# Kernel optimization log

Measured on AMD Instinct MI355X. Metric: run time of the kernel, lower is better.

The kernel has to match this reference:

```python
import jax, jax.numpy as jnp
import numpy as np
from jax import lax


def setup_inputs() -> dict:
    key = jax.random.key(0)
    k1, k2 = jax.random.split(key)
    B, C, H, W = 4, 64, 64, 64
    foreground = jax.random.normal(k1, (B, C, H, W), dtype=jnp.float32)
    masks = jax.random.uniform(k2, (B, 1, H, W), dtype=jnp.float32)
    return {"foreground": foreground, "masks": masks}


def reference(foreground, masks):
    # First-call path of KnowledgeConsistentAttention (att_scores_prev is None).
    # patch_size=3 -> padding=1 around 1x1 dynamic kernels; propagate_size=3 -> 3x3 sum pool.
    B, C, H, W = foreground.shape
    P = H * W
    # Dynamic 1x1 kernels: one per spatial location, L2-normalized over channels.
    K = foreground.reshape(B, C, P).transpose(0, 2, 1)            # [B, P, C]
    norm = jnp.sqrt(jnp.sum(K * K, axis=2, keepdims=True))        # flatten(1).norm per kernel
    K = K / (norm + 1e-8)
    # conv2d with 1x1 kernels and padding=1 == GEMM over zero-padded input.
    Xpad = jnp.pad(foreground, ((0, 0), (0, 0), (1, 1), (1, 1)))  # [B, C, H+2, W+2]
    scores = jnp.einsum('bpc,bchw->bphw', K, Xpad)                # [B, P, H+2, W+2]
    # avg_pool2d(k=3, stride=1, pad=1) * 9 == zero-padded 3x3 sum pool.
    scores = lax.reduce_window(scores, jnp.float32(0.0), lax.add,
                               (1, 1, 3, 3), (1, 1, 1, 1), 'SAME')
    attn = jax.nn.softmax(scores, axis=1)                          # softmax over P kernels
    # conv_transpose2d with 1x1 kernels, padding=1 crops the border back to HxW.
    out = jnp.einsum('bphw,bpc->bchw', attn[:, :, 1:-1, 1:-1], K)  # [B, C, H, W]
    return out
```

## Files before the change

kernel.cpp:

```cpp
#include <hip/hip_runtime.h>
#include <hip/hip_bf16.h>
#include <math.h>

#define Bn 4
#define Cn 64
#define Pn 4096
#define QT 32
#define PBK 128
#define NITER (Pn / PBK)
#define LOG2E 1.4426950408889634f

typedef __attribute__((ext_vector_type(8))) short short8;
typedef __attribute__((ext_vector_type(4))) float float4v;
typedef unsigned short bfu;

__device__ __forceinline__ bfu f2bf(float x) {
    unsigned u = __float_as_uint(x);
    u = (u + 0x7fffu + ((u >> 16) & 1u)) >> 16;
    return (bfu)u;
}

__device__ __forceinline__ void async_load16(const bfu* g, bfu* l) {
    __builtin_amdgcn_global_load_lds(
        (const __attribute__((address_space(1))) unsigned int*)(const void*)g,
        (__attribute__((address_space(3))) unsigned int*)(void*)l,
        16, 0, 0);
}

__global__ __launch_bounds__(256) void prep_kernel(const float* __restrict__ fg,
                                                   bfu* __restrict__ Kpc,
                                                   bfu* __restrict__ Kcp,
                                                   float* __restrict__ S) {
    __shared__ float shbuf[64 * 64];
    int t = threadIdx.x;
    if (blockIdx.x < 512) {
        float* tile  = shbuf;
        float* rnorm = shbuf + 64 * 33;
        int b  = blockIdx.x >> 7;
        int p0 = (blockIdx.x & 127) << 5;
        const float* src = fg + (size_t)b * Cn * Pn + p0;
        #pragma unroll
        for (int i = 0; i < 8; ++i) {
            int idx = i * 256 + t;
            int c = idx >> 5, p = idx & 31;
            tile[c * 33 + p] = src[(size_t)c * Pn + p];
        }
        __syncthreads();
        if (t < 32) {
            float ss = 0.f;
            #pragma unroll
            for (int c = 0; c < 64; ++c) { float v = tile[c * 33 + t]; ss += v * v; }
            rnorm[t] = 1.0f / (sqrtf(ss) + 1e-8f);
        }
        __syncthreads();
        bfu* dpc = Kpc + ((size_t)b * Pn + p0) * Cn;
        #pragma unroll
        for (int i = 0; i < 8; ++i) {
            int idx = i * 256 + t;
            int p = idx >> 6, c = idx & 63;
            dpc[(size_t)p * Cn + c] = f2bf(tile[c * 33 + p] * rnorm[p]);
        }
        bfu* dcp = Kcp + (size_t)b * Cn * Pn + p0;
        #pragma unroll
        for (int i = 0; i < 8; ++i) {
            int idx = i * 256 + t;
            int c = idx >> 5, p = idx & 31;
            dcp[(size_t)c * Pn + p] = f2bf(tile[c * 33 + p] * rnorm[p]);
        }
    } else {
        float (*pl)[64] = (float(*)[64])shbuf;
        int bc = blockIdx.x - 512;
        const float* src = fg + (size_t)bc * Pn;
        float*       dst = S  + (size_t)bc * Pn;
        #pragma unroll
        for (int i = 0; i < 16; ++i) {
            int idx = i * 256 + t;
            pl[idx >> 6][idx & 63] = src[idx];
        }
        __syncthreads();
        #pragma unroll
        for (int i = 0; i < 16; ++i) {
            int idx = i * 256 + t;
            int h = idx >> 6, w = idx & 63;
            float s = 0.f;
            #pragma unroll
            for (int dh = -1; dh <= 1; ++dh) {
                int hh = h + dh;
                if (hh < 0 || hh >= 64) continue;
                #pragma unroll
                for (int dw = -1; dw <= 1; ++dw) {
                    int ww = w + dw;
                    if (ww < 0 || ww >= 64) continue;
                    s += pl[hh][ww];
                }
            }
            dst[idx] = s * LOG2E;
        }
    }
}

__global__ __launch_bounds__(512, 4) void flash_kernel(const bfu* __restrict__ Kpc,
                                                       const bfu* __restrict__ Kcp,
                                                       const float* __restrict__ S,
                                                       float* __restrict__ out) {
    __shared__ __align__(16) bfu smem[26624];
    __shared__ float wredl[8][QT];
    bfu* Sl = smem + 16384;

    int b  = blockIdx.x >> 7;
    int q0 = (blockIdx.x & 127) * QT;
    int t  = threadIdx.x;
    int w = t >> 6, l = t & 63, lq = l & 15, quad = l >> 4;
    int cw = w & 1;
    int kq = w >> 1;

    const float* Sg  = S   + (size_t)b * Cn * Pn;
    const bfu*   gpc = Kpc + (size_t)b * Pn * Cn;
    const bfu*   gcp = Kcp + (size_t)b * Cn * Pn;

    {
        int c = t >> 3, qq = (t & 7) * 4;
        const float* sp = &Sg[(size_t)c * Pn + q0 + qq];
        float4 v0 = *(const float4*)sp;
        float vv[4] = {v0.x, v0.y, v0.z, v0.w};
        int ch = c >> 3, cl = c & 7;
        #pragma unroll
        for (int i = 0; i < 4; ++i) {
            int row = qq + i;
            Sl[row * 64 + ((ch ^ (row & 7)) << 3) + cl] = f2bf(vv[i]);
        }
    }

    #pragma unroll
    for (int pb0 = 0; pb0 < 2; ++pb0) {
        const bfu* gsrc = gpc + (size_t)pb0 * PBK * Cn;
        #pragma unroll
        for (int j = 0; j < 2; ++j) {
            int g = j * 8 + w;
            int ci = g * 64 + l;
            int row = ci >> 3, chp = ci & 7;
            async_load16(gsrc + (size_t)row * Cn + ((chp ^ (row & 7)) << 3),
                         smem + pb0 * 8192 + g * 512);
        }
    }
    __syncthreads();

    short8 bs[2][2];
    #pragma unroll
    for (int nt = 0; nt < 2; ++nt)
        #pragma unroll
        for (int ks = 0; ks < 2; ++ks) {
            int row = nt * 16 + lq;
            bs[nt][ks] = *(const short8*)&Sl[row * 64 + (((ks * 4 + quad) ^ (lq & 7)) << 3)];
        }

    float4v o[2][2];
    #pragma unroll
    for (int ct = 0; ct < 2; ++ct)
        #pragma unroll
        for (int nt = 0; nt < 2; ++nt) o[ct][nt] = (float4v){0.f, 0.f, 0.f, 0.f};
    float lacc[2] = {0.f, 0.f};

    for (int pb = 0; pb < NITER; ++pb) {
        bfu* KpcC = smem + (pb & 1) * 8192;
        bfu* ElC  = smem + 18432 + (pb & 1) * 4096;

        float4 akr[2];
        #pragma unroll
        for (int ct = 0; ct < 2; ++ct)
            akr[ct] = *(const float4*)&gcp[(size_t)(32 * cw + 16 * ct + lq) * Pn +
                                           pb * PBK + 32 * kq + quad * 8];

        short8 af[2];
        #pragma unroll
        for (int ks = 0; ks < 2; ++ks) {
            int row = w * 16 + lq;
            af[ks] = *(const short8*)&KpcC[row * 64 + (((ks * 4 + quad) ^ (lq & 7)) << 3)];
        }
        float4v sc[2];
        #pragma unroll
        for (int nt = 0; nt < 2; ++nt) {
            float4v acc = (float4v){0.f, 0.f, 0.f, 0.f};
            acc = __builtin_amdgcn_mfma_f32_16x16x32_bf16(af[0], bs[nt][0], acc, 0, 0, 0);
            acc = __builtin_amdgcn_mfma_f32_16x16x32_bf16(af[1], bs[nt][1], acc, 0, 0, 0);
            sc[nt] = acc;
        }

        #pragma unroll
        for (int nt = 0; nt < 2; ++nt) {
            int row = nt * 16 + lq;
            float e0 = __builtin_amdgcn_exp2f(sc[nt][0]);
            float e1 = __builtin_amdgcn_exp2f(sc[nt][1]);
            float e2 = __builtin_amdgcn_exp2f(sc[nt][2]);
            float e3 = __builtin_amdgcn_exp2f(sc[nt][3]);
            lacc[nt] += (e0 + e1) + (e2 + e3);
            __hip_bfloat162 h01 = __float22bfloat162_rn(make_float2(e0, e1));
            __hip_bfloat162 h23 = __float22bfloat162_rn(make_float2(e2, e3));
            uint2 pk = make_uint2(*(unsigned*)&h01, *(unsigned*)&h23);
            int col = w * 16 + quad * 4;
            int ch = (col >> 3) ^ (row & 15), cl = col & 7;
            *(uint2*)&ElC[row * PBK + ch * 8 + cl] = pk;
        }

        __syncthreads();

        if (pb + 2 < NITER) {
            const bfu* gsrc = gpc + (size_t)(pb + 2) * PBK * Cn;
            #pragma unroll
            for (int j = 0; j < 2; ++j) {
                int g = j * 8 + w;
                int ci = g * 64 + l;
                int row = ci >> 3, chp = ci & 7;
                async_load16(gsrc + (size_t)row * Cn + ((chp ^ (row & 7)) << 3),
                             KpcC + g * 512);
            }
        }

        #pragma unroll
        for (int ct = 0; ct < 2; ++ct) {
            short8 ak = *(short8*)&akr[ct];
            #pragma unroll
            for (int nt = 0; nt < 2; ++nt) {
                int rowB = nt * 16 + lq;
                short8 bk = *(const short8*)&ElC[rowB * PBK + (((4 * kq + quad) ^ (rowB & 15)) << 3)];
                o[ct][nt] = __builtin_amdgcn_mfma_f32_16x16x32_bf16(ak, bk, o[ct][nt], 0, 0, 0);
            }
        }
    }

    #pragma unroll
    for (int nt = 0; nt < 2; ++nt) {
        lacc[nt] += __shfl_xor(lacc[nt], 16);
        lacc[nt] += __shfl_xor(lacc[nt], 32);
    }
    if (quad == 0) { wredl[w][lq] = lacc[0]; wredl[w][16 + lq] = lacc[1]; }

    float* Ol = (float*)smem;
    __syncthreads();
    #pragma unroll
    for (int ct = 0; ct < 2; ++ct)
        #pragma unroll
        for (int nt = 0; nt < 2; ++nt)
            #pragma unroll
            for (int r = 0; r < 4; ++r)
                Ol[(kq * 64 + cw * 32 + ct * 16 + quad * 4 + r) * 33 + nt * 16 + lq] = o[ct][nt][r];
    __syncthreads();
    float* og = out + (size_t)b * Cn * Pn;
    #pragma unroll
    for (int i = 0; i < 4; ++i) {
        int idx = i * 512 + t;
        int c = idx >> 5, q = idx & 31;
        float lsum = ((wredl[0][q] + wredl[1][q]) + (wredl[2][q] + wredl[3][q])) +
                     ((wredl[4][q] + wredl[5][q]) + (wredl[6][q] + wredl[7][q]));
        float v = ((Ol[c * 33 + q] + Ol[(64 + c) * 33 + q]) +
                   (Ol[(128 + c) * 33 + q] + Ol[(192 + c) * 33 + q])) / lsum;
        og[(size_t)c * Pn + q0 + q] = v;
    }
}

extern "C" void kernel_launch(void* const* d_in, const int* in_sizes, int n_in,
                              void* d_out, int out_size, void* d_ws, size_t ws_size,
                              hipStream_t stream) {
    const float* fg = (const float*)d_in[0];
    float* out = (float*)d_out;
    bfu*   Kpc = (bfu*)d_ws;
    bfu*   Kcp = Kpc + (size_t)Bn * Pn * Cn;
    float* S   = (float*)(Kcp + (size_t)Bn * Pn * Cn);

    prep_kernel <<<768, 256, 0, stream>>>(fg, Kpc, Kcp, S);
    flash_kernel<<<Bn * 128, 512, 0, stream>>>(Kpc, Kcp, S, out);
}
```

Before: 107.1 us.

## Keep exp tile in registers and feed PV MFMA directly, dropping LDS round trip

The second GEMM is restructured so each wave uses its own exponentiated score fragment directly as the A operand of 16x16x16 MFMAs, removing the per-iteration LDS write of the probability tile and the block-wide barrier. K in [P,C] is now read straight from global into registers. A transposed, tiled copy of K (16-position blocks of 64x16) is streamed into per-wave LDS slots with async loads, waited on via s_waitcnt. Each wave now produces partial outputs over its own P slice, so the epilogue does a two-phase LDS reduction across waves. This trades barrier and LDS traffic for more accumulators and a heavier final reduction.

Measured after the change: 105.8 us. Within noise of the previous version (-1.2%).

```diff
diff --git a/kernel.cpp b/kernel.cpp
--- a/kernel.cpp
+++ b/kernel.cpp
@@ -11,6 +11,7 @@
 #define LOG2E 1.4426950408889634f
 
 typedef __attribute__((ext_vector_type(8))) short short8;
+typedef __attribute__((ext_vector_type(4))) short short4v;
 typedef __attribute__((ext_vector_type(4))) float float4v;
 typedef unsigned short bfu;
 
@@ -29,7 +30,7 @@
 
 __global__ __launch_bounds__(256) void prep_kernel(const float* __restrict__ fg,
                                                    bfu* __restrict__ Kpc,
-                                                   bfu* __restrict__ Kcp,
+                                                   bfu* __restrict__ Kcp2,
                                                    float* __restrict__ S) {
     __shared__ float shbuf[64 * 64];
     int t = threadIdx.x;
@@ -60,12 +61,13 @@
             int p = idx >> 6, c = idx & 63;
             dpc[(size_t)p * Cn + c] = f2bf(tile[c * 33 + p] * rnorm[p]);
         }
-        bfu* dcp = Kcp + (size_t)b * Cn * Pn + p0;
+        bfu* d2 = Kcp2 + ((size_t)b * 256 + (p0 >> 4)) * 1024;
         #pragma unroll
         for (int i = 0; i < 8; ++i) {
             int idx = i * 256 + t;
             int c = idx >> 5, p = idx & 31;
-            dcp[(size_t)c * Pn + p] = f2bf(tile[c * 33 + p] * rnorm[p]);
+            d2[(size_t)(p >> 4) * 1024 + c * 16 + (p & 15)] =
+                f2bf(tile[c * 33 + p] * rnorm[p]);
         }
     } else {
         float (*pl)[64] = (float(*)[64])shbuf;
@@ -100,10 +102,10 @@
 }
 
 __global__ __launch_bounds__(512, 4) void flash_kernel(const bfu* __restrict__ Kpc,
-                                                       const bfu* __restrict__ Kcp,
+                                                       const bfu* __restrict__ Kcp2,
                                                        const float* __restrict__ S,
                                                        float* __restrict__ out) {
-    __shared__ __align__(16) bfu smem[26624];
+    __shared__ __align__(16) bfu smem[18432];
     __shared__ float wredl[8][QT];
     bfu* Sl = smem + 16384;
 
@@ -111,12 +113,10 @@
     int q0 = (blockIdx.x & 127) * QT;
     int t  = threadIdx.x;
     int w = t >> 6, l = t & 63, lq = l & 15, quad = l >> 4;
-    int cw = w & 1;
-    int kq = w >> 1;
-
-    const float* Sg  = S   + (size_t)b * Cn * Pn;
-    const bfu*   gpc = Kpc + (size_t)b * Pn * Cn;
-    const bfu*   gcp = Kcp + (size_t)b * Cn * Pn;
+
+    const float* Sg  = S    + (size_t)b * Cn * Pn;
+    const bfu*   gpc = Kpc  + (size_t)b * Pn * Cn;
+    const bfu*   gt  = Kcp2 + (size_t)b * 256 * 1024;
 
     {
         int c = t >> 3, qq = (t & 7) * 4;
@@ -131,17 +131,11 @@
         }
     }
 
-    #pragma unroll
-    for (int pb0 = 0; pb0 < 2; ++pb0) {
-        const bfu* gsrc = gpc + (size_t)pb0 * PBK * Cn;
-        #pragma unroll
-        for (int j = 0; j < 2; ++j) {
-            int g = j * 8 + w;
-            int ci = g * 64 + l;
-            int row = ci >> 3, chp = ci & 7;
-            async_load16(gsrc + (size_t)row * Cn + ((chp ^ (row & 7)) << 3),
-                         smem + pb0 * 8192 + g * 512);
-        }
+    {
+        const bfu* src = gt + (size_t)w * 1024 + l * 8;
+        bfu* dst = smem + w * 1024;
+        async_load16(src, dst);
+        async_load16(src + 512, dst + 512);
     }
     __syncthreads();
 
@@ -154,77 +148,57 @@
             bs[nt][ks] = *(const short8*)&Sl[row * 64 + (((ks * 4 + quad) ^ (lq & 7)) << 3)];
         }
 
-    float4v o[2][2];
-    #pragma unroll
-    for (int ct = 0; ct < 2; ++ct)
-        #pragma unroll
-        for (int nt = 0; nt < 2; ++nt) o[ct][nt] = (float4v){0.f, 0.f, 0.f, 0.f};
+    float4v o[2][4];
+    #pragma unroll
+    for (int nt = 0; nt < 2; ++nt)
+        #pragma unroll
+        for (int cb = 0; cb < 4; ++cb) o[nt][cb] = (float4v){0.f, 0.f, 0.f, 0.f};
     float lacc[2] = {0.f, 0.f};
 
     for (int pb = 0; pb < NITER; ++pb) {
-        bfu* KpcC = smem + (pb & 1) * 8192;
-        bfu* ElC  = smem + 18432 + (pb & 1) * 4096;
-
-        float4 akr[2];
-        #pragma unroll
-        for (int ct = 0; ct < 2; ++ct)
-            akr[ct] = *(const float4*)&gcp[(size_t)(32 * cw + 16 * ct + lq) * Pn +
-                                           pb * PBK + 32 * kq + quad * 8];
-
-        short8 af[2];
-        #pragma unroll
-        for (int ks = 0; ks < 2; ++ks) {
-            int row = w * 16 + lq;
-            af[ks] = *(const short8*)&KpcC[row * 64 + (((ks * 4 + quad) ^ (lq & 7)) << 3)];
-        }
+        bfu* tile = smem + (pb & 1) * 8192 + w * 1024;
+
+        const bfu* ap = gpc + ((size_t)pb * PBK + 16 * w + lq) * Cn + quad * 8;
+        float4 a0 = *(const float4*)ap;
+        float4 a1 = *(const float4*)(ap + 32);
+
+        if (pb + 1 < NITER) {
+            const bfu* src = gt + ((size_t)(pb + 1) * 8 + w) * 1024 + l * 8;
+            bfu* dst = smem + ((pb + 1) & 1) * 8192 + w * 1024;
+            async_load16(src, dst);
+            async_load16(src + 512, dst + 512);
+        }
+
+        short8 af0 = *(short8*)&a0, af1 = *(short8*)&a1;
         float4v sc[2];
         #pragma unroll
         for (int nt = 0; nt < 2; ++nt) {
             float4v acc = (float4v){0.f, 0.f, 0.f, 0.f};
-            acc = __builtin_amdgcn_mfma_f32_16x16x32_bf16(af[0], bs[nt][0], acc, 0, 0, 0);
-            acc = __builtin_amdgcn_mfma_f32_16x16x32_bf16(af[1], bs[nt][1], acc, 0, 0, 0);
+            acc = __builtin_amdgcn_mfma_f32_16x16x32_bf16(af0, bs[nt][0], acc, 0, 0, 0);
+            acc = __builtin_amdgcn_mfma_f32_16x16x32_bf16(af1, bs[nt][1], acc, 0, 0, 0);
             sc[nt] = acc;
         }
 
+        short4v epk[2];
         #pragma unroll
         for (int nt = 0; nt < 2; ++nt) {
-            int row = nt * 16 + lq;
             float e0 = __builtin_amdgcn_exp2f(sc[nt][0]);
             float e1 = __builtin_amdgcn_exp2f(sc[nt][1]);
             float e2 = __builtin_amdgcn_exp2f(sc[nt][2]);
             float e3 = __builtin_amdgcn_exp2f(sc[nt][3]);
             lacc[nt] += (e0 + e1) + (e2 + e3);
-            __hip_bfloat162 h01 = __float22bfloat162_rn(make_float2(e0, e1));
-            __hip_bfloat162 h23 = __float22bfloat162_rn(make_float2(e2, e3));
-            uint2 pk = make_uint2(*(unsigned*)&h01, *(unsigned*)&h23);
-            int col = w * 16 + quad * 4;
-            int ch = (col >> 3) ^ (row & 15), cl = col & 7;
-            *(uint2*)&ElC[row * PBK + ch * 8 + cl] = pk;
-        }
-
-        __syncthreads();
-
-        if (pb + 2 < NITER) {
-            const bfu* gsrc = gpc + (size_t)(pb + 2) * PBK * Cn;
-            #pragma unroll
-            for (int j = 0; j < 2; ++j) {
-                int g = j * 8 + w;
-                int ci = g * 64 + l;
-                int row = ci >> 3, chp = ci & 7;
-                async_load16(gsrc + (size_t)row * Cn + ((chp ^ (row & 7)) << 3),
-                             KpcC + g * 512);
-            }
-        }
-
-        #pragma unroll
-        for (int ct = 0; ct < 2; ++ct) {
-            short8 ak = *(short8*)&akr[ct];
-            #pragma unroll
-            for (int nt = 0; nt < 2; ++nt) {
-                int rowB = nt * 16 + lq;
-                short8 bk = *(const short8*)&ElC[rowB * PBK + (((4 * kq + quad) ^ (rowB & 15)) << 3)];
-                o[ct][nt] = __builtin_amdgcn_mfma_f32_16x16x32_bf16(ak, bk, o[ct][nt], 0, 0, 0);
-            }
+            short4v ep = {(short)f2bf(e0), (short)f2bf(e1), (short)f2bf(e2), (short)f2bf(e3)};
+            epk[nt] = ep;
+        }
+
+        __builtin_amdgcn_s_waitcnt(0x0F72);
+        __builtin_amdgcn_sched_barrier(0);
+
+        #pragma unroll
+        for (int cb = 0; cb < 4; ++cb) {
+            short4v kb = *(const short4v*)&tile[(16 * cb + lq) * 16 + quad * 4];
+            o[0][cb] = __builtin_amdgcn_mfma_f32_16x16x16bf16_1k(epk[0], kb, o[0][cb], 0, 0, 0);
+            o[1][cb] = __builtin_amdgcn_mfma_f32_16x16x16bf16_1k(epk[1], kb, o[1][cb], 0, 0, 0);
         }
     }
 
@@ -237,14 +211,27 @@
 
     float* Ol = (float*)smem;
     __syncthreads();
-    #pragma unroll
-    for (int ct = 0; ct < 2; ++ct)
+    if (w < 4) {
         #pragma unroll
         for (int nt = 0; nt < 2; ++nt)
             #pragma unroll
-            for (int r = 0; r < 4; ++r)
-                Ol[(kq * 64 + cw * 32 + ct * 16 + quad * 4 + r) * 33 + nt * 16 + lq] = o[ct][nt][r];
-    __syncthreads();
+            for (int cb = 0; cb < 4; ++cb)
+                #pragma unroll
+                for (int r = 0; r < 4; ++r)
+                    Ol[(w * 32 + nt * 16 + quad * 4 + r) * 66 + cb * 16 + lq] = o[nt][cb][r];
+    }
+    __syncthreads();
+    if (w >= 4) {
+        #pragma unroll
+        for (int nt = 0; nt < 2; ++nt)
+            #pragma unroll
+            for (int cb = 0; cb < 4; ++cb)
+                #pragma unroll
+                for (int r = 0; r < 4; ++r)
+                    Ol[((w - 4) * 32 + nt * 16 + quad * 4 + r) * 66 + cb * 16 + lq] += o[nt][cb][r];
+    }
+    __syncthreads();
+
     float* og = out + (size_t)b * Cn * Pn;
     #pragma unroll
     for (int i = 0; i < 4; ++i) {
@@ -252,8 +239,8 @@
         int c = idx >> 5, q = idx & 31;
         float lsum = ((wredl[0][q] + wredl[1][q]) + (wredl[2][q] + wredl[3][q])) +
                      ((wredl[4][q] + wredl[5][q]) + (wredl[6][q] + wredl[7][q]));
-        float v = ((Ol[c * 33 + q] + Ol[(64 + c) * 33 + q]) +
-                   (Ol[(128 + c) * 33 + q] + Ol[(192 + c) * 33 + q])) / lsum;
+        float v = ((Ol[q * 66 + c] + Ol[(32 + q) * 66 + c]) +
+                   (Ol[(64 + q) * 66 + c] + Ol[(96 + q) * 66 + c])) / lsum;
         og[(size_t)c * Pn + q0 + q] = v;
     }
 }
@@ -263,10 +250,10 @@
                               hipStream_t stream) {
     const float* fg = (const float*)d_in[0];
     float* out = (float*)d_out;
-    bfu*   Kpc = (bfu*)d_ws;
-    bfu*   Kcp = Kpc + (size_t)Bn * Pn * Cn;
-    float* S   = (float*)(Kcp + (size_t)Bn * Pn * Cn);
-
-    prep_kernel <<<768, 256, 0, stream>>>(fg, Kpc, Kcp, S);
-    flash_kernel<<<Bn * 128, 512, 0, stream>>>(Kpc, Kcp, S, out);
-}
+    bfu*   Kpc  = (bfu*)d_ws;
+    bfu*   Kcp2 = Kpc + (size_t)Bn * Pn * Cn;
+    float* S    = (float*)(Kcp2 + (size_t)Bn * Pn * Cn);
+
+    prep_kernel <<<768, 256, 0, stream>>>(fg, Kpc, Kcp2, S);
+    flash_kernel<<<Bn * 128, 512, 0, stream>>>(Kpc, Kcp2, S, out);
+}
```
